# Kernel tuning notes

Measured on AMD Instinct MI355X. Metric: run time of the kernel, lower is better.

## Reference

```python
import jax, jax.numpy as jnp
import numpy as np


def setup_inputs() -> dict:
    key = jax.random.key(0)
    k1, k2 = jax.random.split(key)
    B, d, h = 65536, 256, 1024  # na = d//4 = 64, G = B//na = 1024, h = 4*d
    x = jax.random.normal(k1, (B, d), dtype=jnp.float32)
    A = 0.1 * jax.random.normal(k2, (d, h), dtype=jnp.float32)
    return {"x": x, "A": A}


def reference(x, A):
    # x: [B, d], A: [d, h] with h = 4*d, na = d // 4, G = B // na
    B, d = x.shape
    na = d // 4
    G = B // na
    n2 = 2 * na

    # bmm with broadcast A + SiLU -> [B, h]; reshape [B, 16, na], sum -> [B]
    J = jax.nn.silu(x @ A)                      # [B, h]
    j12 = J.reshape(B, 16, na).sum(axis=(1, 2)).reshape(G, na)  # [G, na]

    # kron(diag(j12), eye(2)) duplicates each diagonal entry onto a 2x2 identity
    diagvals = jnp.repeat(j12, 2, axis=1)        # [G, 2*na]

    # Final block matrix [[J11, J12], [J21, J22]] with J11=J22=0,
    # J12 = +diag, J21 = -diag, each expanded by kron with eye(2).
    idx = jnp.arange(n2)
    out = jnp.zeros((G, 4 * na, 4 * na), dtype=x.dtype)
    out = out.at[:, idx, n2 + idx].set(diagvals)    # top-right block diagonal
    out = out.at[:, n2 + idx, idx].set(-diagvals)   # bottom-left block diagonal
    return out
```

## Files before the change

### kernel.cpp

```cpp
#include <hip/hip_runtime.h>
#include <stdint.h>

typedef float    f32x4  __attribute__((ext_vector_type(4)));
typedef __bf16   bf16x8 __attribute__((ext_vector_type(8)));
typedef uint32_t u32x4  __attribute__((ext_vector_type(4)));
typedef unsigned short u16x4 __attribute__((ext_vector_type(4)));

#define AS1 __attribute__((address_space(1)))
#define AS3 __attribute__((address_space(3)))

__device__ __forceinline__ unsigned short f2bf_bits(float f) {
  uint32_t u = __builtin_bit_cast(uint32_t, f);
  u += 0x7fffu + ((u >> 16) & 1u);
  return (unsigned short)(u >> 16);
}

__global__ void k_transpose_cvt(const float* __restrict__ A,
                                unsigned short* __restrict__ At) {
  int n = blockIdx.x * blockDim.x + threadIdx.x;
  int o = n << 2;
  int col = o >> 8;
  int k   = o & 255;
  u16x4 v;
#pragma unroll
  for (int j = 0; j < 4; ++j) v[j] = f2bf_bits(A[(size_t)(k + j) * 1024 + col]);
  *reinterpret_cast<u16x4*>(At + o) = v;
}

__launch_bounds__(256, 2)
__global__ void k_fused(const float* __restrict__ x,
                        const unsigned short* __restrict__ At,
                        float* __restrict__ out) {
  __shared__ alignas(16) char lds[4][8192];

  const int tid  = threadIdx.x;
  const int lane = tid & 63;
  const int w    = tid >> 6;
  const int h    = w & 1;
  const int g    = blockIdx.x * 2 + (w >> 1);

  const int col = lane & 15;
  const int hi  = lane >> 4;

  uint32_t p0  = (uint32_t)((w * 2 + 0) * 1024 + lane * 16);
  uint32_t so0 = p0 ^ (((p0 >> 9) & 7u) << 4);
  uint32_t p1  = (uint32_t)((w * 2 + 1) * 1024 + lane * 16);
  uint32_t so1 = p1 ^ (((p1 >> 9) & 7u) << 4);
  const uint32_t d0 = (uint32_t)(w * 2 + 0) * 1024;
  const uint32_t d1 = (uint32_t)(w * 2 + 1) * 1024;

#pragma unroll
  for (int t = 0; t < 2; ++t) {
    const char* src = (const char*)At + (size_t)t * 8192;
    __builtin_amdgcn_global_load_lds((const AS1 uint32_t*)(src + so0),
                                     (AS3 uint32_t*)(lds[t] + d0), 16, 0, 0);
    __builtin_amdgcn_global_load_lds((const AS1 uint32_t*)(src + so1),
                                     (AS3 uint32_t*)(lds[t] + d1), 16, 0, 0);
  }
  __builtin_amdgcn_sched_barrier(0);

  bf16x8 xf[2][8];
#pragma unroll
  for (int r = 0; r < 2; ++r) {
    const float* xr = x + (size_t)(g * 64 + h * 32 + r * 16 + col) * 256;
#pragma unroll
    for (int s = 0; s < 8; ++s) {
      f32x4 a = __builtin_nontemporal_load(
          reinterpret_cast<const f32x4*>(xr + s * 32 + hi * 8));
      f32x4 bq = __builtin_nontemporal_load(
          reinterpret_cast<const f32x4*>(xr + s * 32 + hi * 8 + 4));
      bf16x8 f;
      f[0] = (__bf16)a[0];  f[1] = (__bf16)a[1];
      f[2] = (__bf16)a[2];  f[3] = (__bf16)a[3];
      f[4] = (__bf16)bq[0]; f[5] = (__bf16)bq[1];
      f[6] = (__bf16)bq[2]; f[7] = (__bf16)bq[3];
      xf[r][s] = f;
    }
  }
  asm volatile("s_waitcnt vmcnt(0)\n\ts_barrier" ::: "memory");

  uint32_t rbase = ((uint32_t)(col * 512 + hi * 16)) ^ ((uint32_t)(col & 7) << 4);

  float sums[2][4] = {{0.f,0.f,0.f,0.f},{0.f,0.f,0.f,0.f}};
  float* og = out + (size_t)g * 65536;
  float* fillbase = og + (size_t)h * 32768 + lane * 4;
  const f32x4 z4 = {0.f, 0.f, 0.f, 0.f};

  for (int t = 0; t < 64; ++t) {
    {
      int pt = (t + 2) & 63;
      const char* src = (const char*)At + (size_t)pt * 8192;
      char* dst = lds[(t + 2) & 3];
      __builtin_amdgcn_global_load_lds((const AS1 uint32_t*)(src + so0),
                                       (AS3 uint32_t*)(dst + d0), 16, 0, 0);
      __builtin_amdgcn_global_load_lds((const AS1 uint32_t*)(src + so1),
                                       (AS3 uint32_t*)(dst + d1), 16, 0, 0);
    }
    __builtin_amdgcn_sched_barrier(0);
    {
      float* zp = fillbase + t * 512;
      __builtin_nontemporal_store(z4, reinterpret_cast<f32x4*>(zp));
      __builtin_nontemporal_store(z4, reinterpret_cast<f32x4*>(zp + 256));
    }
    asm volatile("s_waitcnt vmcnt(10)\n\ts_barrier" ::: "memory");

    const char* buf = lds[t & 3];
    bf16x8 bfr[8];
#pragma unroll
    for (int s = 0; s < 8; ++s) {
      uint32_t addr = rbase ^ ((uint32_t)s << 6);
      bfr[s] = __builtin_bit_cast(
          bf16x8, *reinterpret_cast<const u32x4*>(buf + addr));
    }
    f32x4 a00 = {0.f,0.f,0.f,0.f}, a01 = {0.f,0.f,0.f,0.f};
    f32x4 a10 = {0.f,0.f,0.f,0.f}, a11 = {0.f,0.f,0.f,0.f};
#pragma unroll
    for (int s = 0; s < 4; ++s) {
      a00 = __builtin_amdgcn_mfma_f32_16x16x32_bf16(xf[0][s],     bfr[s],     a00, 0, 0, 0);
      a01 = __builtin_amdgcn_mfma_f32_16x16x32_bf16(xf[0][s + 4], bfr[s + 4], a01, 0, 0, 0);
      a10 = __builtin_amdgcn_mfma_f32_16x16x32_bf16(xf[1][s],     bfr[s],     a10, 0, 0, 0);
      a11 = __builtin_amdgcn_mfma_f32_16x16x32_bf16(xf[1][s + 4], bfr[s + 4], a11, 0, 0, 0);
    }
#pragma unroll
    for (int j = 0; j < 4; ++j) {
      float z0 = a00[j] + a01[j];
      float z1 = a10[j] + a11[j];
      float s0 = __builtin_amdgcn_rcpf(1.0f + __expf(-z0));
      float s1 = __builtin_amdgcn_rcpf(1.0f + __expf(-z1));
      sums[0][j] += z0 * s0;
      sums[1][j] += z1 * s1;
    }
  }

  asm volatile("s_waitcnt vmcnt(0)\n\ts_barrier" ::: "memory");

#pragma unroll
  for (int r = 0; r < 2; ++r)
#pragma unroll
    for (int j = 0; j < 4; ++j) {
      float v = sums[r][j];
      v += __shfl_xor(v, 1, 64);
      v += __shfl_xor(v, 2, 64);
      v += __shfl_xor(v, 4, 64);
      v += __shfl_xor(v, 8, 64);
      sums[r][j] = v;
    }

  if (col == 0) {
#pragma unroll
    for (int r = 0; r < 2; ++r)
#pragma unroll
      for (int j = 0; j < 4; ++j) {
        int c = h * 32 + r * 16 + hi * 4 + j;
        float s = sums[r][j];
        og[(2 * c) * 256 + 128 + 2 * c]     =  s;
        og[(2 * c + 1) * 256 + 129 + 2 * c] =  s;
        og[(128 + 2 * c) * 256 + 2 * c]     = -s;
        og[(129 + 2 * c) * 256 + 2 * c + 1] = -s;
      }
  }
}

extern "C" void kernel_launch(void* const* d_in, const int* in_sizes, int n_in,
                              void* d_out, int out_size, void* d_ws, size_t ws_size,
                              hipStream_t stream) {
  const float* x = (const float*)d_in[0];
  const float* A = (const float*)d_in[1];
  float* out = (float*)d_out;
  unsigned short* At = (unsigned short*)d_ws;

  k_transpose_cvt<<<256, 256, 0, stream>>>(A, At);
  k_fused<<<512, 256, 0, stream>>>(x, At, out);
}
```

Baseline: 82.05 us.

## Split fused kernel into single-wave blocks and move diagonal writes to a separate kernel

Changes the fused GEMM+SiLU kernel from 4-wave blocks sharing a 4-deep LDS ring to independent 1-wave blocks, each staging its own full 8KB B tile through a 2-buffer LDS double-buffer without s_barrier. Zero-fill of the output is interleaved as before, but the last chunks are issued up front. Diagonal writes move to a separate small kernel reading j12 from workspace, which avoids races between the zero-fill and the diagonal stores across blocks. The cost is 4x more redundant At traffic per wave, one extra launch, and tighter vmcnt bookkeeping.

```diff
diff --git a/kernel.cpp b/kernel.cpp
--- a/kernel.cpp
+++ b/kernel.cpp
@@ -27,36 +27,32 @@
   *reinterpret_cast<u16x4*>(At + o) = v;
 }
 
-__launch_bounds__(256, 2)
+__launch_bounds__(64, 2)
 __global__ void k_fused(const float* __restrict__ x,
                         const unsigned short* __restrict__ At,
-                        float* __restrict__ out) {
-  __shared__ alignas(16) char lds[4][8192];
-
-  const int tid  = threadIdx.x;
-  const int lane = tid & 63;
-  const int w    = tid >> 6;
-  const int h    = w & 1;
-  const int g    = blockIdx.x * 2 + (w >> 1);
+                        float* __restrict__ out,
+                        float* __restrict__ j12) {
+  __shared__ alignas(16) char lds[2][8192];
+
+  const int lane = threadIdx.x;
+  const int b    = blockIdx.x;
+  const int g    = b >> 1;
+  const int h    = b & 1;
 
   const int col = lane & 15;
   const int hi  = lane >> 4;
 
-  uint32_t p0  = (uint32_t)((w * 2 + 0) * 1024 + lane * 16);
-  uint32_t so0 = p0 ^ (((p0 >> 9) & 7u) << 4);
-  uint32_t p1  = (uint32_t)((w * 2 + 1) * 1024 + lane * 16);
-  uint32_t so1 = p1 ^ (((p1 >> 9) & 7u) << 4);
-  const uint32_t d0 = (uint32_t)(w * 2 + 0) * 1024;
-  const uint32_t d1 = (uint32_t)(w * 2 + 1) * 1024;
-
-#pragma unroll
-  for (int t = 0; t < 2; ++t) {
-    const char* src = (const char*)At + (size_t)t * 8192;
-    __builtin_amdgcn_global_load_lds((const AS1 uint32_t*)(src + so0),
-                                     (AS3 uint32_t*)(lds[t] + d0), 16, 0, 0);
-    __builtin_amdgcn_global_load_lds((const AS1 uint32_t*)(src + so1),
-                                     (AS3 uint32_t*)(lds[t] + d1), 16, 0, 0);
-  }
+  uint32_t soff[8];
+#pragma unroll
+  for (int i = 0; i < 8; ++i) {
+    uint32_t p = (uint32_t)(i * 1024 + lane * 16);
+    soff[i] = p ^ (((p >> 9) & 7u) << 4);
+  }
+
+#pragma unroll
+  for (int i = 0; i < 8; ++i)
+    __builtin_amdgcn_global_load_lds((const AS1 uint32_t*)((const char*)At + soff[i]),
+                                     (AS3 uint32_t*)(lds[0] + i * 1024), 16, 0, 0);
   __builtin_amdgcn_sched_barrier(0);
 
   bf16x8 xf[2][8];
@@ -77,34 +73,24 @@
       xf[r][s] = f;
     }
   }
-  asm volatile("s_waitcnt vmcnt(0)\n\ts_barrier" ::: "memory");
-
-  uint32_t rbase = ((uint32_t)(col * 512 + hi * 16)) ^ ((uint32_t)(col & 7) << 4);
-
-  float sums[2][4] = {{0.f,0.f,0.f,0.f},{0.f,0.f,0.f,0.f}};
+  __builtin_amdgcn_sched_barrier(0);
+
   float* og = out + (size_t)g * 65536;
   float* fillbase = og + (size_t)h * 32768 + lane * 4;
   const f32x4 z4 = {0.f, 0.f, 0.f, 0.f};
 
-  for (int t = 0; t < 64; ++t) {
-    {
-      int pt = (t + 2) & 63;
-      const char* src = (const char*)At + (size_t)pt * 8192;
-      char* dst = lds[(t + 2) & 3];
-      __builtin_amdgcn_global_load_lds((const AS1 uint32_t*)(src + so0),
-                                       (AS3 uint32_t*)(dst + d0), 16, 0, 0);
-      __builtin_amdgcn_global_load_lds((const AS1 uint32_t*)(src + so1),
-                                       (AS3 uint32_t*)(dst + d1), 16, 0, 0);
-    }
-    __builtin_amdgcn_sched_barrier(0);
-    {
-      float* zp = fillbase + t * 512;
-      __builtin_nontemporal_store(z4, reinterpret_cast<f32x4*>(zp));
-      __builtin_nontemporal_store(z4, reinterpret_cast<f32x4*>(zp + 256));
-    }
-    asm volatile("s_waitcnt vmcnt(10)\n\ts_barrier" ::: "memory");
-
-    const char* buf = lds[t & 3];
+#pragma unroll
+  for (int c = 60; c < 64; ++c) {
+    float* zp = fillbase + c * 512;
+    __builtin_nontemporal_store(z4, reinterpret_cast<f32x4*>(zp));
+    __builtin_nontemporal_store(z4, reinterpret_cast<f32x4*>(zp + 256));
+  }
+  asm volatile("s_waitcnt vmcnt(0)" ::: "memory");
+
+  uint32_t rbase = ((uint32_t)(col * 512 + hi * 16)) ^ ((uint32_t)(col & 7) << 4);
+  float sums[2][4] = {{0.f,0.f,0.f,0.f},{0.f,0.f,0.f,0.f}};
+
+  auto do_tile = [&](const char* buf) {
     bf16x8 bfr[8];
 #pragma unroll
     for (int s = 0; s < 8; ++s) {
@@ -130,9 +116,42 @@
       sums[0][j] += z0 * s0;
       sums[1][j] += z1 * s1;
     }
-  }
-
-  asm volatile("s_waitcnt vmcnt(0)\n\ts_barrier" ::: "memory");
+  };
+  auto stage = [&](int t) {
+    const char* src = (const char*)At + (size_t)t * 8192;
+    char* dst = lds[t & 1];
+#pragma unroll
+    for (int i = 0; i < 8; ++i)
+      __builtin_amdgcn_global_load_lds((const AS1 uint32_t*)(src + soff[i]),
+                                       (AS3 uint32_t*)(dst + i * 1024), 16, 0, 0);
+  };
+
+  for (int t = 0; t < 60; ++t) {
+    asm volatile("s_waitcnt lgkmcnt(0)" ::: "memory");
+    stage(t + 1);
+    __builtin_amdgcn_sched_barrier(0);
+    {
+      float* zp = fillbase + t * 512;
+      __builtin_nontemporal_store(z4, reinterpret_cast<f32x4*>(zp));
+      __builtin_nontemporal_store(z4, reinterpret_cast<f32x4*>(zp + 256));
+    }
+    asm volatile("s_waitcnt vmcnt(12)" ::: "memory");
+    do_tile(lds[t & 1]);
+  }
+  asm volatile("s_waitcnt lgkmcnt(0)" ::: "memory");
+  stage(61);
+  asm volatile("s_waitcnt vmcnt(10)" ::: "memory");
+  do_tile(lds[0]);
+  asm volatile("s_waitcnt lgkmcnt(0)" ::: "memory");
+  stage(62);
+  asm volatile("s_waitcnt vmcnt(8)" ::: "memory");
+  do_tile(lds[1]);
+  asm volatile("s_waitcnt lgkmcnt(0)" ::: "memory");
+  stage(63);
+  asm volatile("s_waitcnt vmcnt(8)" ::: "memory");
+  do_tile(lds[0]);
+  asm volatile("s_waitcnt vmcnt(0)" ::: "memory");
+  do_tile(lds[1]);
 
 #pragma unroll
   for (int r = 0; r < 2; ++r)
@@ -145,20 +164,26 @@
       v += __shfl_xor(v, 8, 64);
       sums[r][j] = v;
     }
-
   if (col == 0) {
 #pragma unroll
     for (int r = 0; r < 2; ++r)
 #pragma unroll
-      for (int j = 0; j < 4; ++j) {
-        int c = h * 32 + r * 16 + hi * 4 + j;
-        float s = sums[r][j];
-        og[(2 * c) * 256 + 128 + 2 * c]     =  s;
-        og[(2 * c + 1) * 256 + 129 + 2 * c] =  s;
-        og[(128 + 2 * c) * 256 + 2 * c]     = -s;
-        og[(129 + 2 * c) * 256 + 2 * c + 1] = -s;
-      }
-  }
+      for (int j = 0; j < 4; ++j)
+        j12[g * 64 + h * 32 + r * 16 + hi * 4 + j] = sums[r][j];
+  }
+}
+
+__global__ void k_diag(const float* __restrict__ j12,
+                       float* __restrict__ out) {
+  int t = blockIdx.x * 256 + threadIdx.x;
+  int g = t >> 6;
+  int c = t & 63;
+  float s = j12[t];
+  float* og = out + (size_t)g * 65536;
+  og[(2 * c) * 256 + 128 + 2 * c]     =  s;
+  og[(2 * c + 1) * 256 + 129 + 2 * c] =  s;
+  og[(128 + 2 * c) * 256 + 2 * c]     = -s;
+  og[(129 + 2 * c) * 256 + 2 * c + 1] = -s;
 }
 
 extern "C" void kernel_launch(void* const* d_in, const int* in_sizes, int n_in,
@@ -168,7 +193,9 @@
   const float* A = (const float*)d_in[1];
   float* out = (float*)d_out;
   unsigned short* At = (unsigned short*)d_ws;
+  float* j12 = (float*)((char*)d_ws + 512 * 1024);
 
   k_transpose_cvt<<<256, 256, 0, stream>>>(A, At);
-  k_fused<<<512, 256, 0, stream>>>(x, At, out);
-}
+  k_fused<<<2048, 64, 0, stream>>>(x, At, out, j12);
+  k_diag<<<256, 256, 0, stream>>>(j12, out);
+}
```

Result: slower. 87.89 us (+7.1%).
